# Kernel optimization log

Hardware: AMD Instinct MI355X
Metric: run time of the kernel (lower is better)

The kernel has to match this reference:

```python
import jax, jax.numpy as jnp
import numpy as np

B, NV, HID, TDIM = 1024, 256, 256, 128
NODE_IN = 2 + 4 + TDIM  # coords + pos_enc(4) + time_emb


def _sinusoidal_pos_emb(t, dim):
    # standard SinusoidalPosEmb: cat(sin, cos) of t * exp(-i*log(1e4)/(half-1))
    half = dim // 2
    freqs = jnp.exp(-np.log(10000.0) * jnp.arange(half, dtype=t.dtype) / (half - 1))
    ang = t[:, None] * freqs[None, :]
    return jnp.concatenate([jnp.sin(ang), jnp.cos(ang)], axis=-1)  # [B, dim]


def setup_inputs() -> dict:
    key = jax.random.key(0)
    ks = jax.random.split(key, 10)
    s = lambda fan_in: 1.0 / np.sqrt(fan_in)
    return {
        "x": jax.random.normal(ks[0], (B, NV * 2), dtype=jnp.float32),
        "t": jax.random.uniform(ks[1], (B,), dtype=jnp.float32) * 1000.0,
        "time_w": jax.random.normal(ks[2], (TDIM, TDIM), dtype=jnp.float32) * s(TDIM),
        "time_b": jnp.zeros((TDIM,), dtype=jnp.float32),
        "W0": jax.random.normal(ks[3], (NODE_IN, HID), dtype=jnp.float32) * s(NODE_IN),
        "b0": jnp.zeros((HID,), dtype=jnp.float32),
        "W1": jax.random.normal(ks[4], (HID, HID), dtype=jnp.float32) * s(HID),
        "b1": jnp.zeros((HID,), dtype=jnp.float32),
        "W2": jax.random.normal(ks[5], (HID, HID), dtype=jnp.float32) * s(HID),
        "b2": jnp.zeros((HID,), dtype=jnp.float32),
    }


def reference(x, t, time_w, time_b, W0, b0, W1, b1, W2, b2):
    Bsz, D = x.shape
    n = D // 2
    coords = x.reshape(Bsz, n, 2)  # [B, n, 2]

    # cycle positional features (pos_enc_dim=4): sin/cos of vertex angle + 2nd harmonic
    pos = jnp.arange(n, dtype=x.dtype)
    theta = (2.0 * jnp.pi) * pos / n
    pe = jnp.stack([jnp.sin(theta), jnp.cos(theta), jnp.sin(2.0 * theta), jnp.cos(2.0 * theta)], axis=-1)
    pe = jnp.broadcast_to(pe[None], (Bsz, n, 4))

    # time MLP: SinusoidalPosEmb -> Linear -> SiLU, broadcast to every node of the graph
    temb = jax.nn.silu(_sinusoidal_pos_emb(t, time_w.shape[0]) @ time_w + time_b)  # [B, TDIM]
    temb = jnp.broadcast_to(temb[:, None, :], (Bsz, n, temb.shape[-1]))

    h = jnp.concatenate([coords, pe, temb], axis=-1)  # [B, n, NODE_IN]

    # GCN layers over cycle adjacency with self-loops, symmetric-normalized (deg=3 -> 1/3).
    # Cycle structure: neighbors are prev/next vertex within each polygon -> jnp.roll on axis 1.
    for W, b in ((W0, b0), (W1, b1), (W2, b2)):
        s = h @ W + b  # support = x W + b
        agg = (s + jnp.roll(s, 1, axis=1) + jnp.roll(s, -1, axis=1)) / 3.0
        h = jax.nn.silu(agg)

    # mean pooling per graph (scatter_mean over graph_index == mean over vertex axis here)
    return h.mean(axis=1)  # [B, HID]
```

## Files before the change

### kernel.cpp

```cpp
#include <hip/hip_runtime.h>
#include <cstdint>

typedef __attribute__((ext_vector_type(8)))  short bf16x8;
typedef __attribute__((ext_vector_type(16))) float f32x16;
typedef __attribute__((ext_vector_type(2)))  float f32x2;
typedef __attribute__((ext_vector_type(4)))  int   i32x4;

__device__ __forceinline__ unsigned short f2bf(float x) {
  unsigned u = __float_as_uint(x);
  u += 0x7fffu + ((u >> 16) & 1u);
  return (unsigned short)(u >> 16);
}
__device__ __forceinline__ float bf2f(unsigned short h) {
  return __uint_as_float(((unsigned)h) << 16);
}
__device__ __forceinline__ float silu_f(float v) {
  return v * __builtin_amdgcn_rcpf(1.0f + __expf(-v));
}
__device__ __forceinline__ unsigned pk2bf(float lo, float hi) {
#if defined(__has_builtin)
#if __has_builtin(__builtin_amdgcn_cvt_pk_bf16_f32)
  auto v = __builtin_amdgcn_cvt_pk_bf16_f32(lo, hi);
  unsigned u; __builtin_memcpy(&u, &v, 4); return u;
#else
  return ((unsigned)f2bf(hi) << 16) | (unsigned)f2bf(lo);
#endif
#else
  return ((unsigned)f2bf(hi) << 16) | (unsigned)f2bf(lo);
#endif
}
__device__ __forceinline__ unsigned lo_pack(unsigned x, unsigned y) {
  return __builtin_amdgcn_perm(y, x, 0x05040100u);
}
__device__ __forceinline__ unsigned hi_pack(unsigned x, unsigned y) {
  return __builtin_amdgcn_perm(y, x, 0x07060302u);
}

__global__ void pack_kernel(const float* __restrict__ W0, const float* __restrict__ W1,
                            const float* __restrict__ W2,
                            unsigned short* __restrict__ packW) {
  const int idx = blockIdx.x * 256 + threadIdx.x;
  const float* W; int KT, kmax, base, lidx;
  if (idx < 36864)        { W = W0; KT = 9;  kmax = 134; base = 0;      lidx = idx; }
  else if (idx < 102400)  { W = W1; KT = 16; kmax = 256; base = 36864;  lidx = idx - 36864; }
  else                    { W = W2; KT = 16; kmax = 256; base = 102400; lidx = idx - 102400; }
  const int k   = lidx >> 8;
  const int col = lidx & 255;
  const float v = (k < kmax) ? W[k * 256 + col] : 0.0f;
  const int kt = k >> 4, kr = k & 15, q = kr >> 3, j = kr & 7;
  const int g = col >> 6, t = (col >> 5) & 1, n = col & 31;
  const int dest = base + g * (KT * 1024) + t * (KT * 512) + kt * 512 + (q * 32 + n) * 8 + j;
  packW[dest] = f2bf(v);
}

template <int KT, int LAYER>
__device__ __forceinline__ void gcn_layer(
    const int tid, const int w, const int lane, const int q, const int c, const int sig,
    const unsigned short* __restrict__ packL,
    const float* __restrict__ BIAS,
    const bf16x8* Aold, bf16x8* Anew,
    unsigned short* bnd, unsigned int* scr3_w, float* poolw) {
#pragma unroll
  for (int g = 0; g < 4; ++g) {
    const unsigned short* srcg = packL + g * (KT * 1024);

    f32x16 acc0, acc1;
#pragma unroll
    for (int i = 0; i < 16; ++i) { acc0[i] = 0.f; acc1[i] = 0.f; }
    {
      const bf16x8* wb0 = (const bf16x8*)srcg;
      const bf16x8* wb1 = (const bf16x8*)(srcg + KT * 512);
#pragma unroll
      for (int kt = 0; kt < KT; ++kt) {
        bf16x8 b0 = wb0[kt * 64 + lane];
        bf16x8 b1 = wb1[kt * 64 + lane];
        acc0 = __builtin_amdgcn_mfma_f32_32x32x16_bf16(Aold[kt], b0, acc0, 0, 0, 0);
        acc1 = __builtin_amdgcn_mfma_f32_32x32x16_bf16(Aold[kt], b1, acc1, 0, 0, 0);
      }
    }

    unsigned short* bndp = bnd + (g & 1) * 2048;
    if (q == 0) { bndp[(w * 2 + 0) * 64 + c]      = f2bf(acc0[0]);
                  bndp[(w * 2 + 0) * 64 + 32 + c] = f2bf(acc1[0]); }
    else        { bndp[(w * 2 + 1) * 64 + c]      = f2bf(acc0[15]);
                  bndp[(w * 2 + 1) * 64 + 32 + c] = f2bf(acc1[15]); }
    __syncthreads();

    const float e0t0  = __shfl_xor(acc0[0], 32);
    const float e0t1  = __shfl_xor(acc1[0], 32);
    const float e15t0 = __shfl_xor(acc0[15], 32);
    const float e15t1 = __shfl_xor(acc1[15], 32);
    const float bp0 = bf2f(bndp[(((w + 7) & 7) * 2 + 1) * 64 + c]);
    const float bp1 = bf2f(bndp[(((w + 7) & 7) * 2 + 1) * 64 + 32 + c]);
    const float bn0 = bf2f(bndp[(((w + 1) & 7) * 2 + 0) * 64 + c]);
    const float bn1 = bf2f(bndp[(((w + 1) & 7) * 2 + 0) * 64 + 32 + c]);
    const float bias0 = BIAS[g * 64 + c], bias1 = BIAS[g * 64 + 32 + c];
    const float T = 0.33333333333f;
    float ps0 = 0.f, ps1 = 0.f;
#pragma unroll
    for (int r = 0; r < 16; ++r) {
      float pr0, pr1, nx0, nx1;
      if (r > 0)       { pr0 = acc0[r - 1]; pr1 = acc1[r - 1]; }
      else             { pr0 = q ? e15t0 : bp0; pr1 = q ? e15t1 : bp1; }
      if (r < 15)      { nx0 = acc0[r + 1]; nx1 = acc1[r + 1]; }
      else             { nx0 = q ? bn0 : e0t0; nx1 = q ? bn1 : e0t1; }
      f32x2 v2;
      v2.x = (pr0 + acc0[r] + nx0) * T + bias0;
      v2.y = (pr1 + acc1[r] + nx1) * T + bias1;
      f32x2 ex; ex.x = __expf(-v2.x); ex.y = __expf(-v2.y);
      f32x2 den = ex + 1.0f;
      f32x2 y2;
      y2.x = v2.x * __builtin_amdgcn_rcpf(den.x);
      y2.y = v2.y * __builtin_amdgcn_rcpf(den.y);
      if constexpr (LAYER == 2) { ps0 += y2.x; ps1 += y2.y; }
      else {
        scr3_w[(16 * q + r) * 34 + c] = pk2bf(y2.x, y2.y);
      }
    }

    if constexpr (LAYER == 2) {
      ps0 += __shfl_xor(ps0, 32);
      ps1 += __shfl_xor(ps1, 32);
      if (q == 0) { poolw[w * 256 + g * 64 + c]      = ps0;
                    poolw[w * 256 + g * 64 + 32 + c] = ps1; }
    } else {
      const unsigned int* sb = scr3_w + sig * 34;
      uint2 d0 = *(const uint2*)(sb + 8 * q + 0);
      uint2 d1 = *(const uint2*)(sb + 8 * q + 2);
      uint2 d2 = *(const uint2*)(sb + 8 * q + 4);
      uint2 d3 = *(const uint2*)(sb + 8 * q + 6);
      uint2 e0 = *(const uint2*)(sb + 16 + 8 * q + 0);
      uint2 e1 = *(const uint2*)(sb + 16 + 8 * q + 2);
      uint2 e2 = *(const uint2*)(sb + 16 + 8 * q + 4);
      uint2 e3 = *(const uint2*)(sb + 16 + 8 * q + 6);
      i32x4 f0 = { (int)lo_pack(d0.x, d0.y), (int)lo_pack(d1.x, d1.y),
                   (int)lo_pack(d2.x, d2.y), (int)lo_pack(d3.x, d3.y) };
      i32x4 f1 = { (int)lo_pack(e0.x, e0.y), (int)lo_pack(e1.x, e1.y),
                   (int)lo_pack(e2.x, e2.y), (int)lo_pack(e3.x, e3.y) };
      i32x4 f2v = { (int)hi_pack(d0.x, d0.y), (int)hi_pack(d1.x, d1.y),
                    (int)hi_pack(d2.x, d2.y), (int)hi_pack(d3.x, d3.y) };
      i32x4 f3 = { (int)hi_pack(e0.x, e0.y), (int)hi_pack(e1.x, e1.y),
                   (int)hi_pack(e2.x, e2.y), (int)hi_pack(e3.x, e3.y) };
      Anew[g * 4 + 0] = __builtin_bit_cast(bf16x8, f0);
      Anew[g * 4 + 1] = __builtin_bit_cast(bf16x8, f1);
      Anew[g * 4 + 2] = __builtin_bit_cast(bf16x8, f2v);
      Anew[g * 4 + 3] = __builtin_bit_cast(bf16x8, f3);
    }
  }
}

__global__ __launch_bounds__(512, 2) void poly_kernel(
    const float* __restrict__ x, const float* __restrict__ t,
    const float* __restrict__ tw, const float* __restrict__ tb,
    const unsigned short* __restrict__ packW,
    const float* __restrict__ B0, const float* __restrict__ B1,
    const float* __restrict__ B2, float* __restrict__ out) {
  __shared__ __align__(16) unsigned short bnd[4096];
  __shared__ __align__(16) unsigned int   scr3[8 * 1088];
  __shared__ __align__(16) unsigned short temb_sh[160];

  const int tid = threadIdx.x;
  const int w = tid >> 6, lane = tid & 63;
  const int q = lane >> 5, c = lane & 31;
  const int b = blockIdx.x;
  const int sig = (c & 3) + 4 * ((c >> 3) & 3) + 16 * ((c >> 2) & 1);

  {
    float* e_sh = (float*)bnd;
    float* part = (float*)scr3;
    if (tid < 128) {
      const float tv = t[b];
      const int i = tid & 63;
      const float f = expf(-0.14619588396823767f * (float)i);
      const float ang = tv * f;
      e_sh[tid] = (tid < 64) ? sinf(ang) : cosf(ang);
    }
    __syncthreads();
    {
      const int j = tid & 127, p = tid >> 7;
      float a = 0.f;
#pragma unroll 8
      for (int kk = 0; kk < 32; ++kk) {
        const int k = p * 32 + kk;
        a += e_sh[k] * tw[k * 128 + j];
      }
      part[tid] = a;
    }
    __syncthreads();
    if (tid < 128) {
      const float a = tb[tid] + part[tid] + part[128 + tid] + part[256 + tid] + part[384 + tid];
      temb_sh[6 + tid] = f2bf(silu_f(a));
      if (tid < 6)  temb_sh[tid] = 0;
      if (tid < 10) temb_sh[134 + tid] = 0;
    }
    __syncthreads();
  }

  bf16x8 A0[9], A1[16], A2[16];
  {
#pragma unroll
    for (int kt = 0; kt < 9; ++kt)
      A0[kt] = *(const bf16x8*)(temb_sh + kt * 16 + q * 8);
    if (q == 0) {
      const int n = w * 32 + sig;
      const float2 xy = ((const float2*)x)[b * 256 + n];
      const float th = 0.024543692605870074f * (float)n;
      A0[0][0] = (short)f2bf(xy.x);
      A0[0][1] = (short)f2bf(xy.y);
      A0[0][2] = (short)f2bf(sinf(th));
      A0[0][3] = (short)f2bf(cosf(th));
      A0[0][4] = (short)f2bf(sinf(2.f * th));
      A0[0][5] = (short)f2bf(cosf(2.f * th));
    }
  }

  unsigned int* scr3_w = scr3 + w * 1088;
  float* poolw = (float*)scr3;
  gcn_layer< 9, 0>(tid, w, lane, q, c, sig, packW,          B0, A0, A1, bnd, scr3_w, poolw);
  gcn_layer<16, 1>(tid, w, lane, q, c, sig, packW + 36864,  B1, A1, A2, bnd, scr3_w, poolw);
  gcn_layer<16, 2>(tid, w, lane, q, c, sig, packW + 102400, B2, A2, A1, bnd, scr3_w, poolw);

  __syncthreads();
  if (tid < 256) {
    float s = 0.f;
#pragma unroll
    for (int ww = 0; ww < 8; ++ww) s += poolw[ww * 256 + tid];
    out[b * 256 + tid] = s * (1.f / 256.f);
  }
}

extern "C" void kernel_launch(void* const* d_in, const int* in_sizes, int n_in,
                              void* d_out, int out_size, void* d_ws, size_t ws_size,
                              hipStream_t stream) {
  const float* x  = (const float*)d_in[0];
  const float* t  = (const float*)d_in[1];
  const float* tw = (const float*)d_in[2];
  const float* tb = (const float*)d_in[3];
  const float* W0 = (const float*)d_in[4];
  const float* b0 = (const float*)d_in[5];
  const float* W1 = (const float*)d_in[6];
  const float* b1 = (const float*)d_in[7];
  const float* W2 = (const float*)d_in[8];
  const float* b2 = (const float*)d_in[9];

  unsigned short* packW = (unsigned short*)d_ws;
  float* out = (float*)d_out;

  pack_kernel<<<656, 256, 0, stream>>>(W0, W1, W2, packW);
  poly_kernel<<<1024, 512, 0, stream>>>(x, t, tw, tb, packW, b0, b1, b2, out);
}
```

Before: 208.5 us.

## Stage weight tiles into LDS with async double-buffered global loads

```diff
diff --git a/kernel.cpp b/kernel.cpp
--- a/kernel.cpp
+++ b/kernel.cpp
@@ -35,40 +35,71 @@
 __device__ __forceinline__ unsigned hi_pack(unsigned x, unsigned y) {
   return __builtin_amdgcn_perm(y, x, 0x07060302u);
 }
+__device__ __forceinline__ void gl_lds16(const unsigned short* g, unsigned short* l) {
+  __builtin_amdgcn_global_load_lds(
+      (const __attribute__((address_space(1))) unsigned int*)g,
+      (__attribute__((address_space(3))) unsigned int*)l, 16, 0, 0);
+}
+__device__ __forceinline__ void stage(const unsigned short* src, unsigned short* lds_w,
+                                      const int tid, const int w, const int chunks) {
+  for (int it = 0; it * 512 < chunks; ++it) {
+    const int ci = it * 512 + tid;
+    if (ci < chunks)
+      gl_lds16(src + ci * 8, lds_w + (it * 512 + w * 64) * 8);
+  }
+}
 
 __global__ void pack_kernel(const float* __restrict__ W0, const float* __restrict__ W1,
                             const float* __restrict__ W2,
                             unsigned short* __restrict__ packW) {
-  const int idx = blockIdx.x * 256 + threadIdx.x;
-  const float* W; int KT, kmax, base, lidx;
-  if (idx < 36864)        { W = W0; KT = 9;  kmax = 134; base = 0;      lidx = idx; }
-  else if (idx < 102400)  { W = W1; KT = 16; kmax = 256; base = 36864;  lidx = idx - 36864; }
-  else                    { W = W2; KT = 16; kmax = 256; base = 102400; lidx = idx - 102400; }
-  const int k   = lidx >> 8;
-  const int col = lidx & 255;
-  const float v = (k < kmax) ? W[k * 256 + col] : 0.0f;
-  const int kt = k >> 4, kr = k & 15, q = kr >> 3, j = kr & 7;
-  const int g = col >> 6, t = (col >> 5) & 1, n = col & 31;
-  const int dest = base + g * (KT * 1024) + t * (KT * 512) + kt * 512 + (q * 32 + n) * 8 + j;
-  packW[dest] = f2bf(v);
+  __shared__ float ldsF[16][257];
+  const int s = blockIdx.x, tid = threadIdx.x;
+  const float* W; int KT, kmax, base, kt;
+  if (s < 9)       { W = W0; KT = 9;  kmax = 134; base = 0;      kt = s; }
+  else if (s < 25) { W = W1; KT = 16; kmax = 256; base = 36864;  kt = s - 9; }
+  else             { W = W2; KT = 16; kmax = 256; base = 102400; kt = s - 25; }
+  const int k0 = kt * 16;
+#pragma unroll
+  for (int i = 0; i < 8; ++i) {
+    const int idx = i * 512 + tid;
+    const int kl = idx >> 8, col = idx & 255;
+    const int kg = k0 + kl;
+    ldsF[kl][col] = (kg < kmax) ? W[kg * 256 + col] : 0.0f;
+  }
+  __syncthreads();
+  const int g = tid >> 7, t = (tid >> 6) & 1, lane = tid & 63;
+  const int col = g * 64 + t * 32 + (lane & 31);
+  const int kb = 8 * (lane >> 5);
+  unsigned u0 = pk2bf(ldsF[kb + 0][col], ldsF[kb + 1][col]);
+  unsigned u1 = pk2bf(ldsF[kb + 2][col], ldsF[kb + 3][col]);
+  unsigned u2 = pk2bf(ldsF[kb + 4][col], ldsF[kb + 5][col]);
+  unsigned u3 = pk2bf(ldsF[kb + 6][col], ldsF[kb + 7][col]);
+  unsigned short* dst = packW + base + g * (KT * 1024) + t * (KT * 512) + kt * 512 + lane * 8;
+  i32x4 v = { (int)u0, (int)u1, (int)u2, (int)u3 };
+  *(i32x4*)dst = v;
 }
 
 template <int KT, int LAYER>
 __device__ __forceinline__ void gcn_layer(
     const int tid, const int w, const int lane, const int q, const int c, const int sig,
     const unsigned short* __restrict__ packL,
+    const unsigned short* __restrict__ nextL, const int nextChunks,
     const float* __restrict__ BIAS,
     const bf16x8* Aold, bf16x8* Anew,
-    unsigned short* bnd, unsigned int* scr3_w, float* poolw) {
+    unsigned short* wbuf, unsigned short* bnd,
+    unsigned int* scr3_w, float* poolw) {
 #pragma unroll
   for (int g = 0; g < 4; ++g) {
+    if (g < 3)           stage(packL + (g + 1) * (KT * 1024), wbuf + ((g + 1) & 1) * 8192,
+                               tid, w, KT * 64);
+    else if (nextChunks) stage(nextL, wbuf + ((g + 1) & 1) * 8192, tid, w, nextChunks);
+
     const unsigned short* srcg = packL + g * (KT * 1024);
-
     f32x16 acc0, acc1;
 #pragma unroll
     for (int i = 0; i < 16; ++i) { acc0[i] = 0.f; acc1[i] = 0.f; }
     {
-      const bf16x8* wb0 = (const bf16x8*)srcg;
+      const bf16x8* wb0 = (const bf16x8*)(wbuf + (g & 1) * 8192);
       const bf16x8* wb1 = (const bf16x8*)(srcg + KT * 512);
 #pragma unroll
       for (int kt = 0; kt < KT; ++kt) {
@@ -155,6 +186,7 @@
     const unsigned short* __restrict__ packW,
     const float* __restrict__ B0, const float* __restrict__ B1,
     const float* __restrict__ B2, float* __restrict__ out) {
+  __shared__ __align__(16) unsigned short wbuf[2 * 8192];
   __shared__ __align__(16) unsigned short bnd[4096];
   __shared__ __align__(16) unsigned int   scr3[8 * 1088];
   __shared__ __align__(16) unsigned short temb_sh[160];
@@ -164,6 +196,8 @@
   const int q = lane >> 5, c = lane & 31;
   const int b = blockIdx.x;
   const int sig = (c & 3) + 4 * ((c >> 3) & 3) + 16 * ((c >> 2) & 1);
+
+  stage(packW, wbuf, tid, w, 9 * 64);
 
   {
     float* e_sh = (float*)bnd;
@@ -216,9 +250,12 @@
 
   unsigned int* scr3_w = scr3 + w * 1088;
   float* poolw = (float*)scr3;
-  gcn_layer< 9, 0>(tid, w, lane, q, c, sig, packW,          B0, A0, A1, bnd, scr3_w, poolw);
-  gcn_layer<16, 1>(tid, w, lane, q, c, sig, packW + 36864,  B1, A1, A2, bnd, scr3_w, poolw);
-  gcn_layer<16, 2>(tid, w, lane, q, c, sig, packW + 102400, B2, A2, A1, bnd, scr3_w, poolw);
+  gcn_layer< 9, 0>(tid, w, lane, q, c, sig, packW,          packW + 36864,  16 * 64,
+                   B0, A0, A1, wbuf, bnd, scr3_w, poolw);
+  gcn_layer<16, 1>(tid, w, lane, q, c, sig, packW + 36864,  packW + 102400, 16 * 64,
+                   B1, A1, A2, wbuf, bnd, scr3_w, poolw);
+  gcn_layer<16, 2>(tid, w, lane, q, c, sig, packW + 102400, nullptr,        0,
+                   B2, A2, A1, wbuf, bnd, scr3_w, poolw);
 
   __syncthreads();
   if (tid < 256) {
@@ -246,6 +283,6 @@
   unsigned short* packW = (unsigned short*)d_ws;
   float* out = (float*)d_out;
 
-  pack_kernel<<<656, 256, 0, stream>>>(W0, W1, W2, packW);
+  pack_kernel<<<41, 512, 0, stream>>>(W0, W1, W2, packW);
   poly_kernel<<<1024, 512, 0, stream>>>(x, t, tw, tb, packW, b0, b1, b2, out);
 }
```

After: 214.0 us. 2.6% more time.

## Switch GCN layers to 16x16x32 MFMA with 16 waves per graph

Applied to the files above, without the earlier changes.

```diff
diff --git a/kernel.cpp b/kernel.cpp
--- a/kernel.cpp
+++ b/kernel.cpp
@@ -1,10 +1,9 @@
 #include <hip/hip_runtime.h>
 #include <cstdint>
 
-typedef __attribute__((ext_vector_type(8)))  short bf16x8;
-typedef __attribute__((ext_vector_type(16))) float f32x16;
-typedef __attribute__((ext_vector_type(2)))  float f32x2;
-typedef __attribute__((ext_vector_type(4)))  int   i32x4;
+typedef __attribute__((ext_vector_type(8))) short bf16x8;
+typedef __attribute__((ext_vector_type(4))) float f32x4;
+typedef __attribute__((ext_vector_type(4))) int   i32x4;
 
 __device__ __forceinline__ unsigned short f2bf(float x) {
   unsigned u = __float_as_uint(x);
@@ -39,131 +38,136 @@
 __global__ void pack_kernel(const float* __restrict__ W0, const float* __restrict__ W1,
                             const float* __restrict__ W2,
                             unsigned short* __restrict__ packW) {
-  const int idx = blockIdx.x * 256 + threadIdx.x;
-  const float* W; int KT, kmax, base, lidx;
-  if (idx < 36864)        { W = W0; KT = 9;  kmax = 134; base = 0;      lidx = idx; }
-  else if (idx < 102400)  { W = W1; KT = 16; kmax = 256; base = 36864;  lidx = idx - 36864; }
-  else                    { W = W2; KT = 16; kmax = 256; base = 102400; lidx = idx - 102400; }
-  const int k   = lidx >> 8;
-  const int col = lidx & 255;
-  const float v = (k < kmax) ? W[k * 256 + col] : 0.0f;
-  const int kt = k >> 4, kr = k & 15, q = kr >> 3, j = kr & 7;
-  const int g = col >> 6, t = (col >> 5) & 1, n = col & 31;
-  const int dest = base + g * (KT * 1024) + t * (KT * 512) + kt * 512 + (q * 32 + n) * 8 + j;
-  packW[dest] = f2bf(v);
+  __shared__ float ldsF[32][257];
+  const int s = blockIdx.x, tid = threadIdx.x;
+  const float* W; int KT, kmax, base, kt;
+  if (s < 5)       { W = W0; KT = 5; kmax = 134; base = 0;      kt = s; }
+  else if (s < 13) { W = W1; KT = 8; kmax = 256; base = 40960;  kt = s - 5; }
+  else             { W = W2; KT = 8; kmax = 256; base = 106496; kt = s - 13; }
+#pragma unroll
+  for (int i = 0; i < 16; ++i) {
+    const int idx = i * 512 + tid;
+    const int kl = idx >> 8, col = idx & 255;
+    const int kg = kt * 32 + kl;
+    ldsF[kl][col] = (kg < kmax) ? W[kg * 256 + col] : 0.0f;
+  }
+  __syncthreads();
+#pragma unroll
+  for (int half = 0; half < 2; ++half) {
+    const int f = half * 512 + tid;
+    const int g = f >> 8, nt = (f >> 6) & 3, l = f & 63;
+    const int col = g * 64 + nt * 16 + (l & 15);
+    const int kb = (l >> 4) * 8;
+    i32x4 v = { (int)pk2bf(ldsF[kb + 0][col], ldsF[kb + 1][col]),
+                (int)pk2bf(ldsF[kb + 2][col], ldsF[kb + 3][col]),
+                (int)pk2bf(ldsF[kb + 4][col], ldsF[kb + 5][col]),
+                (int)pk2bf(ldsF[kb + 6][col], ldsF[kb + 7][col]) };
+    *(i32x4*)(packW + base + g * (KT * 2048) + kt * 2048 + nt * 512 + l * 8) = v;
+  }
 }
 
 template <int KT, int LAYER>
 __device__ __forceinline__ void gcn_layer(
-    const int tid, const int w, const int lane, const int q, const int c, const int sig,
-    const unsigned short* __restrict__ packL,
-    const float* __restrict__ BIAS,
+    const int w, const int lane, const int Q, const int cl,
+    const int up, const int dn,
+    const unsigned short* __restrict__ packL, const float* __restrict__ BIAS,
     const bf16x8* Aold, bf16x8* Anew,
-    unsigned short* bnd, unsigned int* scr3_w, float* poolw) {
-#pragma unroll
-  for (int g = 0; g < 4; ++g) {
-    const unsigned short* srcg = packL + g * (KT * 1024);
-
-    f32x16 acc0, acc1;
-#pragma unroll
-    for (int i = 0; i < 16; ++i) { acc0[i] = 0.f; acc1[i] = 0.f; }
-    {
-      const bf16x8* wb0 = (const bf16x8*)srcg;
-      const bf16x8* wb1 = (const bf16x8*)(srcg + KT * 512);
-#pragma unroll
-      for (int kt = 0; kt < KT; ++kt) {
-        bf16x8 b0 = wb0[kt * 64 + lane];
-        bf16x8 b1 = wb1[kt * 64 + lane];
-        acc0 = __builtin_amdgcn_mfma_f32_32x32x16_bf16(Aold[kt], b0, acc0, 0, 0, 0);
-        acc1 = __builtin_amdgcn_mfma_f32_32x32x16_bf16(Aold[kt], b1, acc1, 0, 0, 0);
+    unsigned short* bnd, unsigned int* scrw, float* poolw) {
+  const float T = 0.33333333333f;
+#pragma unroll
+  for (int h = 0; h < 2; ++h) {
+    const bf16x8* wbase = (const bf16x8*)packL;
+    f32x4 acc[8];
+#pragma unroll
+    for (int n8 = 0; n8 < 8; ++n8)
+#pragma unroll
+      for (int r = 0; r < 4; ++r) acc[n8][r] = 0.f;
+#pragma unroll
+    for (int kt = 0; kt < KT; ++kt) {
+#pragma unroll
+      for (int n8 = 0; n8 < 8; ++n8) {
+        const int g = 2 * h + (n8 >> 2), nt = n8 & 3;
+        bf16x8 bf = wbase[(g * KT + kt) * 256 + nt * 64 + lane];
+        acc[n8] = __builtin_amdgcn_mfma_f32_16x16x32_bf16(Aold[kt], bf, acc[n8], 0, 0, 0);
       }
     }
 
-    unsigned short* bndp = bnd + (g & 1) * 2048;
-    if (q == 0) { bndp[(w * 2 + 0) * 64 + c]      = f2bf(acc0[0]);
-                  bndp[(w * 2 + 0) * 64 + 32 + c] = f2bf(acc1[0]); }
-    else        { bndp[(w * 2 + 1) * 64 + c]      = f2bf(acc0[15]);
-                  bndp[(w * 2 + 1) * 64 + 32 + c] = f2bf(acc1[15]); }
-    __syncthreads();
-
-    const float e0t0  = __shfl_xor(acc0[0], 32);
-    const float e0t1  = __shfl_xor(acc1[0], 32);
-    const float e15t0 = __shfl_xor(acc0[15], 32);
-    const float e15t1 = __shfl_xor(acc1[15], 32);
-    const float bp0 = bf2f(bndp[(((w + 7) & 7) * 2 + 1) * 64 + c]);
-    const float bp1 = bf2f(bndp[(((w + 7) & 7) * 2 + 1) * 64 + 32 + c]);
-    const float bn0 = bf2f(bndp[(((w + 1) & 7) * 2 + 0) * 64 + c]);
-    const float bn1 = bf2f(bndp[(((w + 1) & 7) * 2 + 0) * 64 + 32 + c]);
-    const float bias0 = BIAS[g * 64 + c], bias1 = BIAS[g * 64 + 32 + c];
-    const float T = 0.33333333333f;
-    float ps0 = 0.f, ps1 = 0.f;
-#pragma unroll
-    for (int r = 0; r < 16; ++r) {
-      float pr0, pr1, nx0, nx1;
-      if (r > 0)       { pr0 = acc0[r - 1]; pr1 = acc1[r - 1]; }
-      else             { pr0 = q ? e15t0 : bp0; pr1 = q ? e15t1 : bp1; }
-      if (r < 15)      { nx0 = acc0[r + 1]; nx1 = acc1[r + 1]; }
-      else             { nx0 = q ? bn0 : e0t0; nx1 = q ? bn1 : e0t1; }
-      f32x2 v2;
-      v2.x = (pr0 + acc0[r] + nx0) * T + bias0;
-      v2.y = (pr1 + acc1[r] + nx1) * T + bias1;
-      f32x2 ex; ex.x = __expf(-v2.x); ex.y = __expf(-v2.y);
-      f32x2 den = ex + 1.0f;
-      f32x2 y2;
-      y2.x = v2.x * __builtin_amdgcn_rcpf(den.x);
-      y2.y = v2.y * __builtin_amdgcn_rcpf(den.y);
-      if constexpr (LAYER == 2) { ps0 += y2.x; ps1 += y2.y; }
-      else {
-        scr3_w[(16 * q + r) * 34 + c] = pk2bf(y2.x, y2.y);
+    unsigned short* bndp = bnd + (h & 1) * 4096;
+    if (Q == 0) {
+#pragma unroll
+      for (int n8 = 0; n8 < 8; ++n8)
+        bndp[(w * 2 + 0) * 128 + n8 * 16 + cl] = f2bf(acc[n8][0]);
+    } else if (Q == 3) {
+#pragma unroll
+      for (int n8 = 0; n8 < 8; ++n8)
+        bndp[(w * 2 + 1) * 128 + n8 * 16 + cl] = f2bf(acc[n8][3]);
+    }
+    __syncthreads();
+
+    auto comp = [&](int n8, float* y) {
+      float nxt = __shfl(acc[n8][0], up);
+      float prv = __shfl(acc[n8][3], dn);
+      if (Q == 0) prv = bf2f(bndp[(((w + 15) & 15) * 2 + 1) * 128 + n8 * 16 + cl]);
+      if (Q == 3) nxt = bf2f(bndp[(((w + 1) & 15) * 2 + 0) * 128 + n8 * 16 + cl]);
+      const float bias = BIAS[h * 128 + n8 * 16 + cl];
+      const float v0 = (prv        + acc[n8][0] + acc[n8][1]) * T + bias;
+      const float v1 = (acc[n8][0] + acc[n8][1] + acc[n8][2]) * T + bias;
+      const float v2 = (acc[n8][1] + acc[n8][2] + acc[n8][3]) * T + bias;
+      const float v3 = (acc[n8][2] + acc[n8][3] + nxt)        * T + bias;
+      y[0] = silu_f(v0); y[1] = silu_f(v1); y[2] = silu_f(v2); y[3] = silu_f(v3);
+    };
+#pragma unroll
+    for (int cg = 0; cg < 2; ++cg) {
+      if constexpr (LAYER == 2) {
+#pragma unroll
+        for (int t = 0; t < 4; ++t) {
+          float y[4];
+          comp(cg * 4 + t, y);
+          float s = y[0] + y[1] + y[2] + y[3];
+          s += __shfl_xor(s, 16);
+          s += __shfl_xor(s, 32);
+          if (lane < 16) poolw[w * 256 + h * 128 + (cg * 4 + t) * 16 + lane] = s;
+        }
+      } else {
+#pragma unroll
+        for (int t = 0; t < 2; ++t) {
+          float ya[4], yb[4];
+          comp(cg * 4 + t, ya);
+          comp(cg * 4 + t + 2, yb);
+#pragma unroll
+          for (int r = 0; r < 4; ++r)
+            scrw[(4 * Q + r) * 36 + t * 16 + cl] = pk2bf(ya[r], yb[r]);
+        }
+        const unsigned int* sb = scrw + cl * 36;
+        uint4 da = *(const uint4*)(sb + 8 * Q);
+        uint4 db = *(const uint4*)(sb + 8 * Q + 4);
+        i32x4 lo = { (int)lo_pack(da.x, da.y), (int)lo_pack(da.z, da.w),
+                     (int)lo_pack(db.x, db.y), (int)lo_pack(db.z, db.w) };
+        i32x4 hi = { (int)hi_pack(da.x, da.y), (int)hi_pack(da.z, da.w),
+                     (int)hi_pack(db.x, db.y), (int)hi_pack(db.z, db.w) };
+        const int ktp = 2 * (2 * h + cg);
+        Anew[ktp]     = __builtin_bit_cast(bf16x8, lo);
+        Anew[ktp + 1] = __builtin_bit_cast(bf16x8, hi);
       }
     }
-
-    if constexpr (LAYER == 2) {
-      ps0 += __shfl_xor(ps0, 32);
-      ps1 += __shfl_xor(ps1, 32);
-      if (q == 0) { poolw[w * 256 + g * 64 + c]      = ps0;
-                    poolw[w * 256 + g * 64 + 32 + c] = ps1; }
-    } else {
-      const unsigned int* sb = scr3_w + sig * 34;
-      uint2 d0 = *(const uint2*)(sb + 8 * q + 0);
-      uint2 d1 = *(const uint2*)(sb + 8 * q + 2);
-      uint2 d2 = *(const uint2*)(sb + 8 * q + 4);
-      uint2 d3 = *(const uint2*)(sb + 8 * q + 6);
-      uint2 e0 = *(const uint2*)(sb + 16 + 8 * q + 0);
-      uint2 e1 = *(const uint2*)(sb + 16 + 8 * q + 2);
-      uint2 e2 = *(const uint2*)(sb + 16 + 8 * q + 4);
-      uint2 e3 = *(const uint2*)(sb + 16 + 8 * q + 6);
-      i32x4 f0 = { (int)lo_pack(d0.x, d0.y), (int)lo_pack(d1.x, d1.y),
-                   (int)lo_pack(d2.x, d2.y), (int)lo_pack(d3.x, d3.y) };
-      i32x4 f1 = { (int)lo_pack(e0.x, e0.y), (int)lo_pack(e1.x, e1.y),
-                   (int)lo_pack(e2.x, e2.y), (int)lo_pack(e3.x, e3.y) };
-      i32x4 f2v = { (int)hi_pack(d0.x, d0.y), (int)hi_pack(d1.x, d1.y),
-                    (int)hi_pack(d2.x, d2.y), (int)hi_pack(d3.x, d3.y) };
-      i32x4 f3 = { (int)hi_pack(e0.x, e0.y), (int)hi_pack(e1.x, e1.y),
-                   (int)hi_pack(e2.x, e2.y), (int)hi_pack(e3.x, e3.y) };
-      Anew[g * 4 + 0] = __builtin_bit_cast(bf16x8, f0);
-      Anew[g * 4 + 1] = __builtin_bit_cast(bf16x8, f1);
-      Anew[g * 4 + 2] = __builtin_bit_cast(bf16x8, f2v);
-      Anew[g * 4 + 3] = __builtin_bit_cast(bf16x8, f3);
-    }
-  }
-}
-
-__global__ __launch_bounds__(512, 2) void poly_kernel(
+  }
+}
+
+__global__ __launch_bounds__(1024, 4) void poly_kernel(
     const float* __restrict__ x, const float* __restrict__ t,
     const float* __restrict__ tw, const float* __restrict__ tb,
     const unsigned short* __restrict__ packW,
     const float* __restrict__ B0, const float* __restrict__ B1,
     const float* __restrict__ B2, float* __restrict__ out) {
-  __shared__ __align__(16) unsigned short bnd[4096];
-  __shared__ __align__(16) unsigned int   scr3[8 * 1088];
+  __shared__ __align__(16) unsigned short bnd[8192];
+  __shared__ __align__(16) unsigned int   scr3[16 * 576];
   __shared__ __align__(16) unsigned short temb_sh[160];
 
   const int tid = threadIdx.x;
   const int w = tid >> 6, lane = tid & 63;
-  const int q = lane >> 5, c = lane & 31;
+  const int Q = lane >> 4, cl = lane & 15;
+  const int up = (lane + 16) & 63, dn = (lane - 16) & 63;
   const int b = blockIdx.x;
-  const int sig = (c & 3) + 4 * ((c >> 3) & 3) + 16 * ((c >> 2) & 1);
 
   {
     float* e_sh = (float*)bnd;
@@ -180,29 +184,32 @@
       const int j = tid & 127, p = tid >> 7;
       float a = 0.f;
 #pragma unroll 8
-      for (int kk = 0; kk < 32; ++kk) {
-        const int k = p * 32 + kk;
+      for (int kk = 0; kk < 16; ++kk) {
+        const int k = p * 16 + kk;
         a += e_sh[k] * tw[k * 128 + j];
       }
-      part[tid] = a;
+      part[p * 128 + j] = a;
     }
     __syncthreads();
     if (tid < 128) {
-      const float a = tb[tid] + part[tid] + part[128 + tid] + part[256 + tid] + part[384 + tid];
+      float a = tb[tid];
+#pragma unroll
+      for (int pp = 0; pp < 8; ++pp) a += part[pp * 128 + tid];
       temb_sh[6 + tid] = f2bf(silu_f(a));
-      if (tid < 6)  temb_sh[tid] = 0;
-      if (tid < 10) temb_sh[134 + tid] = 0;
-    }
-    __syncthreads();
-  }
-
-  bf16x8 A0[9], A1[16], A2[16];
+      if (tid < 6) temb_sh[tid] = 0;
+    } else if (tid < 154) {
+      temb_sh[6 + tid] = 0;
+    }
+    __syncthreads();
+  }
+
+  bf16x8 A0[5], A1[8], A2[8];
   {
 #pragma unroll
-    for (int kt = 0; kt < 9; ++kt)
-      A0[kt] = *(const bf16x8*)(temb_sh + kt * 16 + q * 8);
-    if (q == 0) {
-      const int n = w * 32 + sig;
+    for (int kt = 0; kt < 5; ++kt)
+      A0[kt] = *(const bf16x8*)(temb_sh + kt * 32 + Q * 8);
+    if (Q == 0) {
+      const int n = w * 16 + cl;
       const float2 xy = ((const float2*)x)[b * 256 + n];
       const float th = 0.024543692605870074f * (float)n;
       A0[0][0] = (short)f2bf(xy.x);
@@ -214,17 +221,17 @@
     }
   }
 
-  unsigned int* scr3_w = scr3 + w * 1088;
+  unsigned int* scrw = scr3 + w * 576;
   float* poolw = (float*)scr3;
-  gcn_layer< 9, 0>(tid, w, lane, q, c, sig, packW,          B0, A0, A1, bnd, scr3_w, poolw);
-  gcn_layer<16, 1>(tid, w, lane, q, c, sig, packW + 36864,  B1, A1, A2, bnd, scr3_w, poolw);
-  gcn_layer<16, 2>(tid, w, lane, q, c, sig, packW + 102400, B2, A2, A1, bnd, scr3_w, poolw);
+  gcn_layer<5, 0>(w, lane, Q, cl, up, dn, packW,          B0, A0, A1, bnd, scrw, poolw);
+  gcn_layer<8, 1>(w, lane, Q, cl, up, dn, packW + 40960,  B1, A1, A2, bnd, scrw, poolw);
+  gcn_layer<8, 2>(w, lane, Q, cl, up, dn, packW + 106496, B2, A2, A1, bnd, scrw, poolw);
 
   __syncthreads();
   if (tid < 256) {
     float s = 0.f;
 #pragma unroll
-    for (int ww = 0; ww < 8; ++ww) s += poolw[ww * 256 + tid];
+    for (int ww = 0; ww < 16; ++ww) s += poolw[ww * 256 + tid];
     out[b * 256 + tid] = s * (1.f / 256.f);
   }
 }
@@ -246,6 +253,6 @@
   unsigned short* packW = (unsigned short*)d_ws;
   float* out = (float*)d_out;
 
-  pack_kernel<<<656, 256, 0, stream>>>(W0, W1, W2, packW);
-  poly_kernel<<<1024, 512, 0, stream>>>(x, t, tw, tb, packW, b0, b1, b2, out);
-}
+  pack_kernel<<<21, 512, 0, stream>>>(W0, W1, W2, packW);
+  poly_kernel<<<1024, 1024, 0, stream>>>(x, t, tw, tb, packW, b0, b1, b2, out);
+}
```

Result: slower. 316.1 us (+51.6%).
